# Performance work log

Hardware: AMD Instinct MI355X
Metric: run time of the kernel (lower is better)

The kernel has to match this reference:

```python
import jax, jax.numpy as jnp
import numpy as np

N_ATOMS = 100000
N_CHANNELS = 4
N_EDGES = 6400000
SMEARING = 1.0


def setup_inputs() -> dict:
    key = jax.random.key(0)
    k1, k2, k3 = jax.random.split(key, 3)
    charges = jax.random.normal(k1, (N_ATOMS, N_CHANNELS), dtype=jnp.float32)
    neighbor_indices = jax.random.randint(k2, (N_EDGES, 2), 0, N_ATOMS, dtype=jnp.int64)
    # physical distances strictly positive, typical cutoff-range values
    neighbor_distances = jax.random.uniform(k3, (N_EDGES,), dtype=jnp.float32,
                                            minval=0.5, maxval=6.0)
    return {"charges": charges,
            "neighbor_indices": neighbor_indices,
            "neighbor_distances": neighbor_distances}


def reference(charges, neighbor_indices, neighbor_distances):
    # Short-range Coulomb potential: erfc(r / (sqrt(2)*smearing)) / r
    pot_bare = jax.scipy.special.erfc(
        neighbor_distances / (jnp.sqrt(jnp.float32(2.0)) * SMEARING)
    ) / neighbor_distances  # [E]

    atom_is = neighbor_indices[:, 0]
    atom_js = neighbor_indices[:, 1]

    contrib_is = charges[atom_js] * pot_bare[:, None]  # [E, C]
    potential = jnp.zeros_like(charges).at[atom_is].add(contrib_is)
    # half neighbor list (full_neighbor_list=False): symmetrize
    contrib_js = charges[atom_is] * pot_bare[:, None]
    potential = potential.at[atom_js].add(contrib_js)
    return potential / 2
```

## Files before the change

kernel.cpp:

```cpp
#include <hip/hip_runtime.h>
#include <hip/hip_fp16.h>

#define BLOCK 1024
#define NB_BIN 480
#define KCONS 48
#define RPB (NB_BIN / KCONS)
#define TILE_ATOMS 10000
#define NTILES_MAX 10
#define WPS_MAX 210
#define WPS_PAD 211
#define FB_TILE_ATOMS 10000
#define FB_TILE_FLOATS (FB_TILE_ATOMS * 2)
#define CPX 3
#define CHUNKS 24
#define RSQRT2 0.70710678118654752440f

typedef float v2f __attribute__((ext_vector_type(2)));
typedef unsigned long long ull;

__device__ __forceinline__ void atomic_add2(float* p, float a, float b) {
#if __has_builtin(__builtin_amdgcn_global_atomic_fadd_v2f32)
    v2f v = {a, b};
    __builtin_amdgcn_global_atomic_fadd_v2f32((v2f*)p, v);
#else
    unsafeAtomicAdd(p + 0, a);
    unsafeAtomicAdd(p + 1, b);
#endif
}

__device__ __forceinline__ void agent_store64(ull* p, ull v) {
    __hip_atomic_store(p, v, __ATOMIC_RELAXED, __HIP_MEMORY_SCOPE_AGENT);
}
__device__ __forceinline__ void agent_store32(unsigned int* p, unsigned int v) {
    __hip_atomic_store(p, v, __ATOMIC_RELAXED, __HIP_MEMORY_SCOPE_AGENT);
}

__device__ __forceinline__ float pot_half(float d) {
    float x = d * RSQRT2;
    float t = __builtin_amdgcn_rcpf(fmaf(0.3275911f, x, 1.0f));
    float p = fmaf(t, 0.5307027145f, -0.7265760135f);
    p = fmaf(t, p, 0.7107068705f);
    p = fmaf(t, p, -0.142248368f);
    p = fmaf(t, p, 0.127414796f);
    p *= t;
    return p * __expf(-0.5f * d * d) * __builtin_amdgcn_rcpf(d);
}

__global__ void detect_idx64_kernel(const unsigned int* __restrict__ idx_u32,
                                    int* __restrict__ flag) {
    __shared__ int nonzero;
    if (threadIdx.x == 0) nonzero = 0;
    __syncthreads();
    unsigned int v = idx_u32[2 * (threadIdx.x +   0) + 1]
                   | idx_u32[2 * (threadIdx.x + 256) + 1]
                   | idx_u32[2 * (threadIdx.x + 512) + 1]
                   | idx_u32[2 * (threadIdx.x + 768) + 1];
    if (v != 0u) atomicAdd(&nonzero, 1);
    __syncthreads();
    if (threadIdx.x == 0) *flag = (nonzero == 0) ? 1 : 0;
}


__global__ __launch_bounds__(BLOCK) void bin_kernel(
    const float4* __restrict__ charges, const void* __restrict__ idx,
    const float* __restrict__ dist,
    ull* __restrict__ entries, unsigned int* __restrict__ counts,
    float* __restrict__ out, const int* __restrict__ flag64,
    int n_edges, int nwords, int wps, int cap, int ntiles, int nb)
{
    __shared__ ull maskA[NTILES_MAX][WPS_PAD];
    __shared__ ull maskB[NTILES_MAX][WPS_PAD];
    __shared__ unsigned short wbase[NTILES_MAX][WPS_PAD];
    bool f64 = (*flag64 != 0);
    int b    = blockIdx.x;
    int lane = threadIdx.x & 63;
    int wave = threadIdx.x >> 6;
    ull lt = (1ull << lane) - 1ull;

    for (int wl = wave; wl < wps; wl += BLOCK / 64) {
        int gw = b * wps + wl;
        int ta = -1, tb = -1;
        if (gw < nwords) {
            int e = gw * 64 + lane;
            if (e < n_edges) {
                int a, bb;
                if (f64) { longlong2 w = ((const longlong2*)idx)[e]; a = (int)w.x; bb = (int)w.y; }
                else     { int2      w = ((const int2*)idx)[e];      a = w.x;      bb = w.y; }
                ta = a / TILE_ATOMS; tb = bb / TILE_ATOMS;
            }
        }
        for (int T = 0; T < ntiles; ++T) {
            ull ma = __ballot(ta == T);
            ull mb = __ballot(tb == T);
            if (lane == 0) { maskA[T][wl] = ma; maskB[T][wl] = mb; }
        }
    }
    __syncthreads();

    if ((int)threadIdx.x < ntiles) {
        int T = threadIdx.x;
        unsigned base = 0;
        for (int wl = 0; wl < wps; ++wl) {
            wbase[T][wl] = (unsigned short)base;
            base += (unsigned)(__popcll(maskA[T][wl]) + __popcll(maskB[T][wl]));
        }
        agent_store32(&counts[(size_t)T * nb + b],
                      base < (unsigned)cap ? base : (unsigned)cap);
    }
    __syncthreads();

    for (int wl = wave; wl < wps; wl += BLOCK / 64) {
        int gw = b * wps + wl;
        if (gw >= nwords) continue;
        int e = gw * 64 + lane;
        int a = 0, bb = 0, ta = -1, tb = -1;
        float q = 0.f;
        if (e < n_edges) {
            if (f64) { longlong2 w = ((const longlong2*)idx)[e]; a = (int)w.x; bb = (int)w.y; }
            else     { int2      w = ((const int2*)idx)[e];      a = w.x;      bb = w.y; }
            ta = a / TILE_ATOMS; tb = bb / TILE_ATOMS;
            q = pot_half(dist[e]);
        }
        ull qb = (ull)__half_as_ushort(__float2half(q)) << 32;
        if (ta >= 0) {
            unsigned slot = wbase[ta][wl] + (unsigned)__popcll(maskA[ta][wl] & lt);
            size_t gs = ((size_t)ta * nb + b) * cap + slot;
            if (slot < (unsigned)cap) {
                agent_store64(&entries[gs],
                    qb | (unsigned)(a - ta * TILE_ATOMS) | ((unsigned)bb << 14));
            } else {
                float4 g = charges[bb];
                float* o = out + (size_t)a * 4;
                unsafeAtomicAdd(o + 0, g.x * q); unsafeAtomicAdd(o + 1, g.y * q);
                unsafeAtomicAdd(o + 2, g.z * q); unsafeAtomicAdd(o + 3, g.w * q);
            }
        }
        if (tb >= 0) {
            unsigned slot = wbase[tb][wl] + (unsigned)__popcll(maskA[tb][wl])
                          + (unsigned)__popcll(maskB[tb][wl] & lt);
            size_t gs = ((size_t)tb * nb + b) * cap + slot;
            if (slot < (unsigned)cap) {
                agent_store64(&entries[gs],
                    qb | (unsigned)(bb - tb * TILE_ATOMS) | ((unsigned)a << 14));
            } else {
                float4 g = charges[a];
                float* o = out + (size_t)bb * 4;
                unsafeAtomicAdd(o + 0, g.x * q); unsafeAtomicAdd(o + 1, g.y * q);
                unsafeAtomicAdd(o + 2, g.z * q); unsafeAtomicAdd(o + 3, g.w * q);
            }
        }
    }
}

__global__ __launch_bounds__(BLOCK, 8) void consume_pk(
    const float4* __restrict__ charges,
    const ull* __restrict__ entries, const unsigned int* __restrict__ counts,
    ull* __restrict__ partials, int cap, int nb, unsigned capmagic)
{
    __shared__ __half2 ht[TILE_ATOMS * 2];
    __shared__ unsigned cnts[RPB];
    int k = blockIdx.x % KCONS;
    int t = blockIdx.x / KCONS;
    for (int i = threadIdx.x; i < TILE_ATOMS * 2; i += BLOCK)
        ((unsigned*)ht)[i] = 0u;
    for (int r = threadIdx.x; r < RPB; r += BLOCK)
        cnts[r] = counts[(size_t)t * nb + k * RPB + r];
    __syncthreads();

    const ull* base = entries + ((size_t)t * nb + (size_t)k * RPB) * cap;
    int total = RPB * cap;
    for (int i0 = (int)threadIdx.x * 4; i0 < total; i0 += BLOCK * 4) {
        ulonglong2 eA = *(const ulonglong2*)(base + i0);
        ulonglong2 eB = *(const ulonglong2*)(base + i0 + 2);
        int r   = (int)(((ull)(unsigned)i0 * capmagic) >> 32);
        int pos = i0 - r * cap;
        unsigned cnt = cnts[r];
        #define PROC(J, EV)                                                  \
            if ((unsigned)(pos + J) < cnt) {                                 \
              unsigned lo = (unsigned)(EV);                                  \
              int rel = (int)(lo & 16383u);                                  \
              int other = (int)(lo >> 14);                                   \
              float q = __half2float(__ushort_as_half(                       \
                            (unsigned short)((EV) >> 32)));                  \
              float4 g = charges[other];                                     \
              __half2 h01 = __floats2half2_rn(g.x * q, g.y * q);             \
              __half2 h23 = __floats2half2_rn(g.z * q, g.w * q);             \
              unsafeAtomicAdd(&ht[rel * 2 + 0], h01);                        \
              unsafeAtomicAdd(&ht[rel * 2 + 1], h23); }
        PROC(0, eA.x) PROC(1, eA.y) PROC(2, eB.x) PROC(3, eB.y)
        #undef PROC
    }
    __syncthreads();

    ull* pb = partials + (size_t)blockIdx.x * TILE_ATOMS;
    for (int r = threadIdx.x; r < TILE_ATOMS; r += BLOCK) {
        __half2 x0 = ht[r * 2 + 0], x1 = ht[r * 2 + 1];
        unsigned b0 = *(unsigned*)&x0, b1 = *(unsigned*)&x1;
        agent_store64(&pb[r], (ull)b0 | ((ull)b1 << 32));
    }
}

__global__ __launch_bounds__(256) void reduce_kernel(
    const ull* __restrict__ partials, float* __restrict__ out, int n_atoms)
{
    int a = blockIdx.x * 256 + threadIdx.x;
    if (a >= n_atoms) return;
    int t   = a / TILE_ATOMS;
    int rel = a - t * TILE_ATOMS;
    const ull* base = partials + ((size_t)t * KCONS) * TILE_ATOMS + rel;
    float4 s = make_float4(0.f, 0.f, 0.f, 0.f);
    #pragma unroll
    for (int k = 0; k < KCONS; ++k) {
        ull v = base[(size_t)k * TILE_ATOMS];
        s.x += __half2float(__ushort_as_half((unsigned short)( v        & 0xffff)));
        s.y += __half2float(__ushort_as_half((unsigned short)((v >> 16) & 0xffff)));
        s.z += __half2float(__ushort_as_half((unsigned short)((v >> 32) & 0xffff)));
        s.w += __half2float(__ushort_as_half((unsigned short)( v >> 48)));
    }
    float* o = out + (size_t)a * 4;
    atomic_add2(o + 0, s.x, s.y);
    atomic_add2(o + 2, s.z, s.w);
}


template <bool F64>
__device__ __forceinline__ void scan_chunk(
    const void* __restrict__ idx, const float* __restrict__ dist,
    const float2* __restrict__ charges2, float* __restrict__ tile,
    int tbase, int h, int e0, int e1)
{
    int ec = e0 + ((e1 - e0) & ~3);
    for (int e4 = e0 + (int)threadIdx.x * 4; e4 < ec; e4 += BLOCK * 4) {
        int a[4], b[4];
        if (F64) {
            #pragma unroll
            for (int k = 0; k < 4; ++k) {
                longlong2 w = ((const longlong2*)idx)[e4 + k];
                a[k] = (int)w.x; b[k] = (int)w.y;
            }
        } else {
            int4 w01 = ((const int4*)idx)[(e4 >> 1) + 0];
            int4 w23 = ((const int4*)idx)[(e4 >> 1) + 1];
            a[0] = w01.x; b[0] = w01.y; a[1] = w01.z; b[1] = w01.w;
            a[2] = w23.x; b[2] = w23.y; a[3] = w23.z; b[3] = w23.w;
        }
        float4 dv = *(const float4*)(dist + e4);
        float d[4] = {dv.x, dv.y, dv.z, dv.w};
        float q[4];
        #pragma unroll
        for (int k = 0; k < 4; ++k) q[k] = pot_half(d[k]);
        #pragma unroll
        for (int k = 0; k < 4; ++k) {
            unsigned ri = (unsigned)(a[k] - tbase);
            unsigned rj = (unsigned)(b[k] - tbase);
            if (ri < FB_TILE_ATOMS) {
                float2 g = charges2[b[k] * 2 + h];
                atomicAdd(&tile[ri * 2 + 0], g.x * q[k]);
                atomicAdd(&tile[ri * 2 + 1], g.y * q[k]);
            }
            if (rj < FB_TILE_ATOMS) {
                float2 g = charges2[a[k] * 2 + h];
                atomicAdd(&tile[rj * 2 + 0], g.x * q[k]);
                atomicAdd(&tile[rj * 2 + 1], g.y * q[k]);
            }
        }
    }
    for (int e = ec + (int)threadIdx.x; e < e1; e += BLOCK) {
        int a, b;
        if (F64) { longlong2 w = ((const longlong2*)idx)[e]; a = (int)w.x; b = (int)w.y; }
        else     { int2      w = ((const int2*)idx)[e];      a = w.x;      b = w.y; }
        unsigned ri = (unsigned)(a - tbase), rj = (unsigned)(b - tbase);
        if (ri < FB_TILE_ATOMS || rj < FB_TILE_ATOMS) {
            float q = pot_half(dist[e]);
            if (ri < FB_TILE_ATOMS) {
                float2 g = charges2[b * 2 + h];
                atomicAdd(&tile[ri * 2 + 0], g.x * q);
                atomicAdd(&tile[ri * 2 + 1], g.y * q);
            }
            if (rj < FB_TILE_ATOMS) {
                float2 g = charges2[a * 2 + h];
                atomicAdd(&tile[rj * 2 + 0], g.x * q);
                atomicAdd(&tile[rj * 2 + 1], g.y * q);
            }
        }
    }
}

__global__ __launch_bounds__(BLOCK, 8) void fused_tile_kernel(
    const float2* __restrict__ charges2, const void* __restrict__ idx,
    const float* __restrict__ dist, float* __restrict__ out,
    const int* __restrict__ flag64,
    int n_edges, int n_atoms, int ntiles, int epc)
{
    __shared__ float tile[FB_TILE_FLOATS];
    int x   = blockIdx.x & 7;
    int m   = blockIdx.x >> 3;
    int nth = ntiles * 2;
    int cw  = m / nth;
    int rem = m - cw * nth;
    int t   = rem >> 1;
    int h   = rem & 1;
    int c   = x * CPX + cw;
    int tbase = t * FB_TILE_ATOMS;
    for (int i = threadIdx.x; i < FB_TILE_FLOATS; i += BLOCK) tile[i] = 0.f;
    bool f64 = (*flag64 != 0);
    __syncthreads();

    int e0 = c * epc;
    int e1 = min(n_edges, e0 + epc);
    if (e0 < e1) {
        if (f64) scan_chunk<true >(idx, dist, charges2, tile, tbase, h, e0, e1);
        else     scan_chunk<false>(idx, dist, charges2, tile, tbase, h, e0, e1);
    }
    __syncthreads();

    const float2* src = (const float2*)tile;
    for (int r = threadIdx.x; r < FB_TILE_ATOMS; r += BLOCK) {
        int a = tbase + r;
        if (a >= n_atoms) break;
        float2 v = src[r];
        if (v.x != 0.f || v.y != 0.f)
            atomic_add2(out + (size_t)a * 4 + h * 2, v.x, v.y);
    }
}


extern "C" void kernel_launch(void* const* d_in, const int* in_sizes, int n_in,
                              void* d_out, int out_size, void* d_ws, size_t ws_size,
                              hipStream_t stream) {
    const float4* charges  = (const float4*)d_in[0];
    const float2* charges2 = (const float2*)d_in[0];
    const void*   idx      = d_in[1];
    const float*  dist     = (const float*)d_in[2];
    int n_edges = in_sizes[2];
    int n_atoms = in_sizes[0] / 4;
    int* flag   = (int*)d_ws;

    const size_t CTRL = 1024;
    int nwords = (n_edges + 63) / 64;
    int wps    = (nwords + NB_BIN - 1) / NB_BIN;
    int ntiles = (n_atoms + TILE_ATOMS - 1) / TILE_ATOMS;
    int slice  = wps * 64;
    int cap    = ((slice * 2 / (ntiles > 0 ? ntiles : 1)) * 112 / 100 + 63)
                 & ~63;
    unsigned capmagic = (unsigned)((0x100000000ull + cap - 1) / (unsigned)cap);
    size_t nslots         = (size_t)ntiles * NB_BIN * (size_t)cap;
    size_t counts_bytes   = ((size_t)ntiles * NB_BIN * 4 + 255) & ~(size_t)255;
    size_t entries_bytes  = nslots * 8ull;
    size_t partials_bytes = (size_t)ntiles * KCONS * TILE_ATOMS * 8ull;
    size_t needed = CTRL + counts_bytes + entries_bytes + partials_bytes;
    bool use_binned = (ws_size >= needed) && (ntiles <= NTILES_MAX) &&
                      (wps <= WPS_MAX) && (n_atoms <= (1 << 17)) &&
                      (slice * 2 < 65536);

    (void)hipMemsetAsync(d_out, 0, (size_t)out_size * sizeof(float), stream);
    detect_idx64_kernel<<<1, 256, 0, stream>>>((const unsigned int*)idx, flag);

    if (use_binned) {
        char* p = (char*)d_ws + CTRL;
        unsigned int* counts  = (unsigned int*)p;  p += counts_bytes;
        ull*          entries = (ull*)p;           p += entries_bytes;
        ull*          partials = (ull*)p;
        bin_kernel<<<NB_BIN, BLOCK, 0, stream>>>(
            charges, idx, dist, entries, counts, (float*)d_out, flag,
            n_edges, nwords, wps, cap, ntiles, NB_BIN);
        consume_pk<<<ntiles * KCONS, BLOCK, 0, stream>>>(
            charges, entries, counts, partials, cap, NB_BIN, capmagic);
        reduce_kernel<<<(n_atoms + 255) / 256, 256, 0, stream>>>(
            partials, (float*)d_out, n_atoms);
    } else {
        int ntiles_fb = (n_atoms + FB_TILE_ATOMS - 1) / FB_TILE_ATOMS;
        int epc = (((n_edges + CHUNKS - 1) / CHUNKS) + 3) & ~3;
        fused_tile_kernel<<<ntiles_fb * 2 * CHUNKS, BLOCK, 0, stream>>>(
            charges2, idx, dist, (float*)d_out, flag, n_edges, n_atoms,
            ntiles_fb, epc);
    }
}
```

Baseline: 238.0 us.

## Split binning and consumption into two edge-range phases

The edge range is split into two halves, and each half runs its own bin_kernel and consume_pk pair with separate entries/counts buffers and a separate partials slice. The reduce kernel now sums partials from both phases. The intent is to keep each phase's binned entries smaller so they are more likely to stay cache-resident between binning and consumption. In exchange the code adds extra launches, runs each bin_kernel with fewer blocks (240), doubles the partial buffers the reduce reads, and hardcodes 480 = ntiles*KCONS.

After: 316.8 us. 1.33x slower.

```diff
diff --git a/kernel.cpp b/kernel.cpp
--- a/kernel.cpp
+++ b/kernel.cpp
@@ -2,9 +2,10 @@
 #include <hip/hip_fp16.h>
 
 #define BLOCK 1024
-#define NB_BIN 480
+#define NPHASE 2
+#define NB_PHASE 240
 #define KCONS 48
-#define RPB (NB_BIN / KCONS)
+#define RPB (NB_PHASE / KCONS)
 #define TILE_ATOMS 10000
 #define NTILES_MAX 10
 #define WPS_MAX 210
@@ -66,7 +67,7 @@
     const float* __restrict__ dist,
     ull* __restrict__ entries, unsigned int* __restrict__ counts,
     float* __restrict__ out, const int* __restrict__ flag64,
-    int n_edges, int nwords, int wps, int cap, int ntiles, int nb)
+    int n_edges, int w_begin, int w_end, int wps, int cap, int ntiles, int nb)
 {
     __shared__ ull maskA[NTILES_MAX][WPS_PAD];
     __shared__ ull maskB[NTILES_MAX][WPS_PAD];
@@ -78,9 +79,9 @@
     ull lt = (1ull << lane) - 1ull;
 
     for (int wl = wave; wl < wps; wl += BLOCK / 64) {
-        int gw = b * wps + wl;
+        int gw = w_begin + b * wps + wl;
         int ta = -1, tb = -1;
-        if (gw < nwords) {
+        if (gw < w_end) {
             int e = gw * 64 + lane;
             if (e < n_edges) {
                 int a, bb;
@@ -110,8 +111,8 @@
     __syncthreads();
 
     for (int wl = wave; wl < wps; wl += BLOCK / 64) {
-        int gw = b * wps + wl;
-        if (gw >= nwords) continue;
+        int gw = w_begin + b * wps + wl;
+        if (gw >= w_end) continue;
         int e = gw * 64 + lane;
         int a = 0, bb = 0, ta = -1, tb = -1;
         float q = 0.f;
@@ -207,15 +208,20 @@
     if (a >= n_atoms) return;
     int t   = a / TILE_ATOMS;
     int rel = a - t * TILE_ATOMS;
-    const ull* base = partials + ((size_t)t * KCONS) * TILE_ATOMS + rel;
     float4 s = make_float4(0.f, 0.f, 0.f, 0.f);
     #pragma unroll
-    for (int k = 0; k < KCONS; ++k) {
-        ull v = base[(size_t)k * TILE_ATOMS];
-        s.x += __half2float(__ushort_as_half((unsigned short)( v        & 0xffff)));
-        s.y += __half2float(__ushort_as_half((unsigned short)((v >> 16) & 0xffff)));
-        s.z += __half2float(__ushort_as_half((unsigned short)((v >> 32) & 0xffff)));
-        s.w += __half2float(__ushort_as_half((unsigned short)( v >> 48)));
+    for (int p = 0; p < NPHASE; ++p) {
+        const ull* base = partials
+            + ((size_t)(p * NTILES_MAX * 0 + p) * 480 + (size_t)t * KCONS) * TILE_ATOMS
+            + rel;
+        #pragma unroll
+        for (int k = 0; k < KCONS; ++k) {
+            ull v = base[(size_t)k * TILE_ATOMS];
+            s.x += __half2float(__ushort_as_half((unsigned short)( v        & 0xffff)));
+            s.y += __half2float(__ushort_as_half((unsigned short)((v >> 16) & 0xffff)));
+            s.z += __half2float(__ushort_as_half((unsigned short)((v >> 32) & 0xffff)));
+            s.w += __half2float(__ushort_as_half((unsigned short)( v >> 48)));
+        }
     }
     float* o = out + (size_t)a * 4;
     atomic_add2(o + 0, s.x, s.y);
@@ -338,34 +344,47 @@
 
     const size_t CTRL = 1024;
     int nwords = (n_edges + 63) / 64;
-    int wps    = (nwords + NB_BIN - 1) / NB_BIN;
+    int whalf  = (nwords + NPHASE - 1) / NPHASE;
+    int wps    = (whalf + NB_PHASE - 1) / NB_PHASE;
     int ntiles = (n_atoms + TILE_ATOMS - 1) / TILE_ATOMS;
     int slice  = wps * 64;
     int cap    = ((slice * 2 / (ntiles > 0 ? ntiles : 1)) * 112 / 100 + 63)
                  & ~63;
     unsigned capmagic = (unsigned)((0x100000000ull + cap - 1) / (unsigned)cap);
-    size_t nslots         = (size_t)ntiles * NB_BIN * (size_t)cap;
-    size_t counts_bytes   = ((size_t)ntiles * NB_BIN * 4 + 255) & ~(size_t)255;
-    size_t entries_bytes  = nslots * 8ull;
-    size_t partials_bytes = (size_t)ntiles * KCONS * TILE_ATOMS * 8ull;
-    size_t needed = CTRL + counts_bytes + entries_bytes + partials_bytes;
+    size_t nslots_p       = (size_t)ntiles * NB_PHASE * (size_t)cap;
+    size_t counts_bytes   = ((size_t)ntiles * NB_PHASE * 4 + 255) & ~(size_t)255;
+    size_t entries_bytes  = nslots_p * 8ull;
+    size_t partials_bytes = (size_t)NPHASE * 480 * TILE_ATOMS * 8ull;
+    size_t needed = CTRL + NPHASE * (counts_bytes + entries_bytes) +
+                    partials_bytes;
     bool use_binned = (ws_size >= needed) && (ntiles <= NTILES_MAX) &&
                       (wps <= WPS_MAX) && (n_atoms <= (1 << 17)) &&
-                      (slice * 2 < 65536);
+                      (slice * 2 < 65536) && (ntiles * KCONS == 480);
 
     (void)hipMemsetAsync(d_out, 0, (size_t)out_size * sizeof(float), stream);
     detect_idx64_kernel<<<1, 256, 0, stream>>>((const unsigned int*)idx, flag);
 
     if (use_binned) {
         char* p = (char*)d_ws + CTRL;
-        unsigned int* counts  = (unsigned int*)p;  p += counts_bytes;
-        ull*          entries = (ull*)p;           p += entries_bytes;
-        ull*          partials = (ull*)p;
-        bin_kernel<<<NB_BIN, BLOCK, 0, stream>>>(
-            charges, idx, dist, entries, counts, (float*)d_out, flag,
-            n_edges, nwords, wps, cap, ntiles, NB_BIN);
-        consume_pk<<<ntiles * KCONS, BLOCK, 0, stream>>>(
-            charges, entries, counts, partials, cap, NB_BIN, capmagic);
+        unsigned int* countsP[NPHASE];
+        ull*          entriesP[NPHASE];
+        for (int ph = 0; ph < NPHASE; ++ph) {
+            countsP[ph]  = (unsigned int*)p; p += counts_bytes;
+            entriesP[ph] = (ull*)p;          p += entries_bytes;
+        }
+        ull* partials = (ull*)p;
+
+        for (int ph = 0; ph < NPHASE; ++ph) {
+            int w0 = ph * whalf;
+            int w1 = min(nwords, w0 + whalf);
+            bin_kernel<<<NB_PHASE, BLOCK, 0, stream>>>(
+                charges, idx, dist, entriesP[ph], countsP[ph], (float*)d_out,
+                flag, n_edges, w0, w1, wps, cap, ntiles, NB_PHASE);
+            consume_pk<<<ntiles * KCONS, BLOCK, 0, stream>>>(
+                charges, entriesP[ph], countsP[ph],
+                partials + (size_t)ph * 480 * TILE_ATOMS,
+                cap, NB_PHASE, capmagic);
+        }
         reduce_kernel<<<(n_atoms + 255) / 256, 256, 0, stream>>>(
             partials, (float*)d_out, n_atoms);
     } else {
```
